# Kernel optimization log

Measured on AMD Instinct MI355X. Metric: run time of the kernel, lower is better.

Reference implementation:

```python
import jax, jax.numpy as jnp
import numpy as np

B = 4096          # SDE paths (batch_size)
N = 50            # timesteps
DIM = 1
DIM_W = 1
DT = 0.02         # T = 1.0
SIGMA_C = 0.5     # constant diffusion coefficient sigma(t,y)
H = 64            # MLP hidden width ('Default' architecture)
NHID = 3          # three 64->64 hidden layers after the input layer


def _mlp(t, y, Win, bin_, Whid, bhid, Wout, bout):
    # FCnet([2,64,64,64,64,1]) with Sine activation on concat([t, y])
    h = jnp.sin(jnp.concatenate([t, y], axis=-1) @ Win + bin_)
    for i in range(NHID):
        h = jnp.sin(h @ Whid[i] + bhid[i])
    return h @ Wout + bout


def setup_inputs() -> dict:
    key = jax.random.key(0)
    ks = jax.random.split(key, 16)
    def w(k, shape, fan):
        return jax.random.normal(k, shape, jnp.float32) / np.float32(np.sqrt(fan))
    inp = {}
    for p, i in (("Y", 0), ("q", 8)):
        inp[p + "_Win"] = w(ks[i], (2, H), 2)
        inp[p + "_bin"] = jnp.zeros((H,), jnp.float32)
        inp[p + "_Whid"] = w(ks[i + 1], (NHID, H, H), H)
        inp[p + "_bhid"] = jnp.zeros((NHID, H), jnp.float32)
        inp[p + "_Wout"] = w(ks[i + 2], (H, 1), H)
        inp[p + "_bout"] = jnp.zeros((1,), jnp.float32)
    inp["y0_param"] = jnp.ones((1,), jnp.float32)
    inp["dW"] = jax.random.normal(ks[7], (N, B, DIM_W), jnp.float32)  # unit normals; scaled by sqrt(dt) inside reference
    return inp


def _fbsnn_loss(y0_param, Y_Win, Y_bin, Y_Whid, Y_bhid, Y_Wout, Y_bout,
                q_Win, q_bin, q_Whid, q_bhid, q_Wout, q_bout, dW):
    Y_net = lambda t, y: _mlp(t, y, Y_Win, Y_bin, Y_Whid, Y_bhid, Y_Wout, Y_bout)
    q_net = lambda t, y: _mlp(t, y, q_Win, q_bin, q_Whid, q_bhid, q_Wout, q_bout)

    def Y_and_grad(t, y):
        # autograd.grad(Y, y, ones_like(Y)) -> per-sample dY/dy since Y is [B,1]
        Yv, vjp = jax.vjp(lambda yy: Y_net(t, yy), y)
        return Yv, vjp(jnp.ones_like(Yv))[0]

    dWs = dW * np.float32(np.sqrt(DT))             # [N, B, dim_W]
    t0 = jnp.zeros((B, 1), dW.dtype)
    y0 = jnp.tile(y0_param[None, :], (B, 1))       # y0.repeat(batch,1)
    Y0, dY0 = Y_and_grad(t0, y0)

    def step(carry, dW_n):
        t, y, Yv, dYv, loss = carry
        q = q_net(t, y)                                          # control
        sig = jnp.full((B, DIM, DIM_W), SIGMA_C, dW_n.dtype)     # sigma(t,y)
        y1 = y + q * DT + jnp.einsum('bij,bj->bi', sig, dW_n)    # mu = q
        Z = jnp.einsum('bij,bj->bi', sig, dYv)                   # bmm(sigma, dY)
        t1 = t + DT
        Y1, dY1 = Y_and_grad(t1, y1)
        f = q ** 2                                               # generator(y,q)
        Y1_tilde = Yv - f * DT + Z * dW_n
        loss = loss + jnp.mean((Y1 - Y1_tilde) ** 2)
        return (t1, y1, Y1, dY1, loss), None

    carry0 = (t0, y0, Y0, dY0, jnp.zeros((), dW.dtype))
    (tN, yN, YN, dYN, res_loss), _ = jax.lax.scan(step, carry0, dWs)

    g = lambda yy: jnp.sum(yy ** 2, axis=-1, keepdims=True)      # terminal_cost(y)
    term, vjp_g = jax.vjp(g, yN)
    term_grad = vjp_g(jnp.ones_like(term))[0]
    return (res_loss
            + jnp.mean((YN - term) ** 2)
            + jnp.mean((dYN - term_grad) ** 2))


def reference(y0_param, Y_Win, Y_bin, Y_Whid, Y_bhid, Y_Wout, Y_bout,
              q_Win, q_bin, q_Whid, q_bhid, q_Wout, q_bout, dW):
    return _fbsnn_loss(y0_param, Y_Win, Y_bin, Y_Whid, Y_bhid, Y_Wout, Y_bout,
                       q_Win, q_bin, q_Whid, q_bhid, q_Wout, q_bout, dW)
```

## Files before the change

kernel.cpp:

```cpp
#include <hip/hip_runtime.h>


#define NPATH   4096
#define NSTEP   50
#define DT_F    0.02f
#define SQRT_DT 0.14142136f
#define SIGMA_F 0.5f
#define INV2PI  0.15915494309189535f
#define TWOPI_F 6.28318530717958648f

#define GRID_N   128
#define GRID_INV 8.0f
#define GRID_DY  0.125f

#define NPROD_Q 25
#define NPROD_Y 26
#define NCONS   64
#define NBLK    (51 + NCONS)
#define PPB     64

#define QG_FLOATS  (NSTEP * GRID_N)
#define YD_FLOATS  (2 * (NSTEP + 1) * GRID_N)

#define MAGIC 0x5AB1C0DEu

#define FR_AIN(t)     (t)
#define FR_AH(L,t,kk) (4 + (L)*8 + (t)*2 + (kk))
#define FR_AOUT(kk)   (28 + (kk))
#define FR_BIN(t)     (30 + (t))
#define FR_BHD(L,t)   (34 + (L)*4 + (t))
#define FR_BOUT       46

#define WS_DONE 0
#define WS_QG   64
#define WS_YD   (WS_QG + QG_FLOATS)
#define WS_PAIR (WS_YD + YD_FLOATS)

#define L_QG    0
#define L_YD    QG_FLOATS
#define L_DW    (L_YD + YD_FLOATS)
#define SMEM_FLOATS (L_DW + NSTEP * PPB)
#define SMEM_BYTES  (SMEM_FLOATS * 4)

typedef __attribute__((ext_vector_type(8)))  short s16x8;
typedef __attribute__((ext_vector_type(4)))  float f32x4;
typedef __attribute__((ext_vector_type(4)))  float float4v;
typedef __attribute__((ext_vector_type(2)))  float float2v;

#if __has_builtin(__builtin_amdgcn_cvt_pk_bf16_f32)
__device__ __forceinline__ unsigned pkbf(float a, float b) {
    auto r = __builtin_amdgcn_cvt_pk_bf16_f32(a, b);
    unsigned u; __builtin_memcpy(&u, &r, 4); return u;
}
#else
__device__ __forceinline__ unsigned pkbf(float a, float b) {
    unsigned ua = __float_as_uint(a), ub = __float_as_uint(b);
    ua += 0x7fffu + ((ua >> 16) & 1u);
    ub += 0x7fffu + ((ub >> 16) & 1u);
    return (ua >> 16) | (ub & 0xffff0000u);
}
#endif

__device__ __forceinline__ s16x8 frag4(unsigned a, unsigned b, unsigned c, unsigned d) {
    union { unsigned u[4]; s16x8 s; } x;
    x.u[0] = a; x.u[1] = b; x.u[2] = c; x.u[3] = d;
    return x.s;
}

__device__ __forceinline__ float sinrev(float x) {
#if __has_builtin(__builtin_amdgcn_sinf)
    return __builtin_amdgcn_sinf(x);
#else
    return __sinf(x * TWOPI_F);
#endif
}
__device__ __forceinline__ float cosrev(float x) {
#if __has_builtin(__builtin_amdgcn_cosf)
    return __builtin_amdgcn_cosf(x);
#else
    return __cosf(x * TWOPI_F);
#endif
}

__device__ __forceinline__ int slot16(int t, int r) {
    return (t < 2) ? 8 * (r >> 2) + 4 * t + (r & 3)
                   : 32 + 8 * (r >> 2) + 4 * (t - 2) + (r & 3);
}

__device__ __forceinline__ void build_half(
    int sec, int half, const float* __restrict__ Win, const float* __restrict__ bin,
    const float* __restrict__ Whid, const float* __restrict__ bhid,
    const float* __restrict__ Wout, const float* __restrict__ bo,
    int qd, int m, char* fbl)
{
    const int t0 = 2 * half;
    if (sec == 0) {
#pragma unroll
        for (int t = t0; t < t0 + 2; ++t) {
            const int uo = slot16(t, m);
            unsigned w0 = 0;
            if (qd == 0) w0 = pkbf(INV2PI * Win[uo], INV2PI * Win[64 + uo]);
            *reinterpret_cast<s16x8*>(fbl + FR_AIN(t) * 1024) = frag4(w0, 0u, 0u, 0u);
            f32x4 bi;
#pragma unroll
            for (int i = 0; i < 4; ++i) bi[i] = INV2PI * bin[slot16(t, 4 * qd + i)];
            *reinterpret_cast<f32x4*>(fbl + FR_BIN(t) * 1024) = bi;
        }
        if (half == 0) {
#pragma unroll
            for (int kk = 0; kk < 2; ++kk) {
                unsigned w[4] = {0u, 0u, 0u, 0u};
                if (m == 0) {
#pragma unroll
                    for (int j2 = 0; j2 < 4; ++j2) {
                        int e0 = 32 * kk + 8 * qd + 2 * j2;
                        w[j2] = pkbf(Wout[e0], Wout[e0 + 1]);
                    }
                }
                *reinterpret_cast<s16x8*>(fbl + FR_AOUT(kk) * 1024) = frag4(w[0], w[1], w[2], w[3]);
            }
            f32x4 bo4 = {bo[0], 0.0f, 0.0f, 0.0f};
            *reinterpret_cast<f32x4*>(fbl + FR_BOUT * 1024) = bo4;
        }
    } else {
        const int L = sec - 1;
#pragma unroll
        for (int t = t0; t < t0 + 2; ++t) {
            const int uo = slot16(t, m);
            const float* W = Whid + L * 4096 + uo;
#pragma unroll
            for (int kk = 0; kk < 2; ++kk) {
                unsigned w[4];
#pragma unroll
                for (int j2 = 0; j2 < 4; ++j2) {
                    int e0 = 32 * kk + 8 * qd + 2 * j2;
                    w[j2] = pkbf(INV2PI * W[e0 * 64], INV2PI * W[(e0 + 1) * 64]);
                }
                *reinterpret_cast<s16x8*>(fbl + FR_AH(L, t, kk) * 1024) = frag4(w[0], w[1], w[2], w[3]);
            }
            f32x4 bh;
#pragma unroll
            for (int i = 0; i < 4; ++i) bh[i] = INV2PI * bhid[L * 64 + slot16(t, 4 * qd + i)];
            *reinterpret_cast<f32x4*>(fbl + FR_BHD(L, t) * 1024) = bh;
        }
    }
}

__device__ __forceinline__ void trans16(const f32x4* C, s16x8& B0, s16x8& B1) {
    float a[4][4];
#pragma unroll
    for (int t = 0; t < 4; ++t)
#pragma unroll
        for (int i = 0; i < 4; ++i) a[t][i] = sinrev(C[t][i]);
    B0 = frag4(pkbf(a[0][0], a[0][1]), pkbf(a[0][2], a[0][3]),
               pkbf(a[1][0], a[1][1]), pkbf(a[1][2], a[1][3]));
    B1 = frag4(pkbf(a[2][0], a[2][1]), pkbf(a[2][2], a[2][3]),
               pkbf(a[3][0], a[3][1]), pkbf(a[3][2], a[3][3]));
}

__device__ __forceinline__ void trans16t(const f32x4* Cf, const f32x4* Ct,
                                         s16x8& Bf0, s16x8& Bf1,
                                         s16x8& Bt0, s16x8& Bt1)
{
    float s[4][4], d[4][4];
#pragma unroll
    for (int t = 0; t < 4; ++t)
#pragma unroll
        for (int i = 0; i < 4; ++i) {
            float cf = Cf[t][i];
            s[t][i] = sinrev(cf);
            d[t][i] = cosrev(cf) * (TWOPI_F * Ct[t][i]);
        }
    Bf0 = frag4(pkbf(s[0][0], s[0][1]), pkbf(s[0][2], s[0][3]),
                pkbf(s[1][0], s[1][1]), pkbf(s[1][2], s[1][3]));
    Bf1 = frag4(pkbf(s[2][0], s[2][1]), pkbf(s[2][2], s[2][3]),
                pkbf(s[3][0], s[3][1]), pkbf(s[3][2], s[3][3]));
    Bt0 = frag4(pkbf(d[0][0], d[0][1]), pkbf(d[0][2], d[0][3]),
                pkbf(d[1][0], d[1][1]), pkbf(d[1][2], d[1][3]));
    Bt1 = frag4(pkbf(d[2][0], d[2][1]), pkbf(d[2][2], d[2][3]),
                pkbf(d[3][0], d[3][1]), pkbf(d[3][2], d[3][3]));
}

__device__ __forceinline__ float grid_ylo(const float* __restrict__ y0p) {
    return floorf(y0p[0] * 8.0f) * 0.125f - 8.0f;
}

__device__ __forceinline__ float eval16_q(const char* fbl, const s16x8& Bty) {
    const f32x4 zc = {0.0f, 0.0f, 0.0f, 0.0f};
    f32x4 C[4];
#pragma unroll
    for (int t = 0; t < 4; ++t) {
        const s16x8 a  = *reinterpret_cast<const s16x8*>(fbl + FR_AIN(t) * 1024);
        const f32x4 bi = *reinterpret_cast<const f32x4*>(fbl + FR_BIN(t) * 1024);
        C[t] = __builtin_amdgcn_mfma_f32_16x16x32_bf16(a, Bty, bi, 0, 0, 0);
    }
    s16x8 B0, B1;
    trans16(C, B0, B1);
#pragma unroll
    for (int L = 0; L < 3; ++L) {
#pragma unroll
        for (int t = 0; t < 4; ++t) {
            const s16x8 a0 = *reinterpret_cast<const s16x8*>(fbl + FR_AH(L, t, 0) * 1024);
            const s16x8 a1 = *reinterpret_cast<const s16x8*>(fbl + FR_AH(L, t, 1) * 1024);
            const f32x4 bh = *reinterpret_cast<const f32x4*>(fbl + FR_BHD(L, t) * 1024);
            f32x4 c = __builtin_amdgcn_mfma_f32_16x16x32_bf16(a0, B0, bh, 0, 0, 0);
            C[t]    = __builtin_amdgcn_mfma_f32_16x16x32_bf16(a1, B1, c, 0, 0, 0);
        }
        trans16(C, B0, B1);
    }
    const s16x8 o0 = *reinterpret_cast<const s16x8*>(fbl + FR_AOUT(0) * 1024);
    const s16x8 o1 = *reinterpret_cast<const s16x8*>(fbl + FR_AOUT(1) * 1024);
    f32x4 Co = __builtin_amdgcn_mfma_f32_16x16x32_bf16(o0, B0, zc, 0, 0, 0);
    Co = __builtin_amdgcn_mfma_f32_16x16x32_bf16(o1, B1, Co, 0, 0, 0);
    return Co[0] + *reinterpret_cast<const float*>(fbl + FR_BOUT * 1024);
}

__device__ __forceinline__ void eval16t(const char* fbl, const s16x8& Bty,
                                        const s16x8& Btn, float& Yv, float& dYv) {
    const f32x4 zc = {0.0f, 0.0f, 0.0f, 0.0f};
    f32x4 Cf[4], Ct[4];
#pragma unroll
    for (int t = 0; t < 4; ++t) {
        const s16x8 a  = *reinterpret_cast<const s16x8*>(fbl + FR_AIN(t) * 1024);
        const f32x4 bi = *reinterpret_cast<const f32x4*>(fbl + FR_BIN(t) * 1024);
        Cf[t] = __builtin_amdgcn_mfma_f32_16x16x32_bf16(a, Bty, bi, 0, 0, 0);
        Ct[t] = __builtin_amdgcn_mfma_f32_16x16x32_bf16(a, Btn, zc, 0, 0, 0);
    }
    s16x8 bf0, bf1, bt0, bt1;
    trans16t(Cf, Ct, bf0, bf1, bt0, bt1);
#pragma unroll
    for (int L = 0; L < 3; ++L) {
#pragma unroll
        for (int t = 0; t < 4; ++t) {
            const s16x8 a0 = *reinterpret_cast<const s16x8*>(fbl + FR_AH(L, t, 0) * 1024);
            const s16x8 a1 = *reinterpret_cast<const s16x8*>(fbl + FR_AH(L, t, 1) * 1024);
            const f32x4 bh = *reinterpret_cast<const f32x4*>(fbl + FR_BHD(L, t) * 1024);
            f32x4 c = __builtin_amdgcn_mfma_f32_16x16x32_bf16(a0, bf0, bh, 0, 0, 0);
            Cf[t]   = __builtin_amdgcn_mfma_f32_16x16x32_bf16(a1, bf1, c, 0, 0, 0);
            f32x4 z = __builtin_amdgcn_mfma_f32_16x16x32_bf16(a0, bt0, zc, 0, 0, 0);
            Ct[t]   = __builtin_amdgcn_mfma_f32_16x16x32_bf16(a1, bt1, z, 0, 0, 0);
        }
        trans16t(Cf, Ct, bf0, bf1, bt0, bt1);
    }
    const s16x8 o0 = *reinterpret_cast<const s16x8*>(fbl + FR_AOUT(0) * 1024);
    const s16x8 o1 = *reinterpret_cast<const s16x8*>(fbl + FR_AOUT(1) * 1024);
    f32x4 Cof = __builtin_amdgcn_mfma_f32_16x16x32_bf16(o0, bf0, zc, 0, 0, 0);
    Cof = __builtin_amdgcn_mfma_f32_16x16x32_bf16(o1, bf1, Cof, 0, 0, 0);
    f32x4 Cot = __builtin_amdgcn_mfma_f32_16x16x32_bf16(o0, bt0, zc, 0, 0, 0);
    Cot = __builtin_amdgcn_mfma_f32_16x16x32_bf16(o1, bt1, Cot, 0, 0, 0);
    Yv  = Cof[0] + *reinterpret_cast<const float*>(fbl + FR_BOUT * 1024);
    dYv = Cot[0];
}

__device__ __forceinline__ float cm4(float q0, float q1, float q2, float q3, float fr) {
    return q1 + 0.5f * fr * ((q2 - q0)
             + fr * ((2.0f * q0 - 5.0f * q1 + 4.0f * q2 - q3)
             + fr * (3.0f * (q1 - q2) + q3 - q0)));
}


extern "C" __global__ void __launch_bounds__(1024, 4)
fbsnn_one(const float* __restrict__ Y_Win, const float* __restrict__ Y_bin,
          const float* __restrict__ Y_Whid, const float* __restrict__ Y_bhid,
          const float* __restrict__ Y_Wout, const float* __restrict__ Y_bout,
          const float* __restrict__ q_Win, const float* __restrict__ q_bin,
          const float* __restrict__ q_Whid, const float* __restrict__ q_bhid,
          const float* __restrict__ q_Wout, const float* __restrict__ q_bout,
          const float* __restrict__ y0p, const float* __restrict__ dW,
          float* __restrict__ ws, float* __restrict__ out)
{
    extern __shared__ __align__(16) float sf[];

    int* done = (int*)ws;
    unsigned long long* pairs = (unsigned long long*)(ws + WS_PAIR);

    const int tid = (int)threadIdx.x;
    const int wv  = tid >> 6;
    const int l   = tid & 63;
    const int qd  = l >> 4;
    const int mm  = l & 15;
    const int blk = (int)blockIdx.x;

    const float ylo = grid_ylo(y0p);

    if (blk < 51) {
        const bool is_q = (blk < NPROD_Q);
        char* fbl = (char*)sf + l * 16;

        if (wv < 8) {
            if (is_q)
                build_half(wv >> 1, wv & 1, q_Win, q_bin, q_Whid, q_bhid,
                           q_Wout, q_bout, qd, mm, fbl);
            else
                build_half(wv >> 1, wv & 1, Y_Win, Y_bin, Y_Whid, Y_bhid,
                           Y_Wout, Y_bout, qd, mm, fbl);
        }
        __syncthreads();

        const int rib  = wv >> 3;
        const int colg = wv & 7;
        const int col  = 16 * colg + mm;
        const int n    = is_q ? (2 * blk + rib) : (2 * (blk - NPROD_Q) + rib);
        const bool valid = is_q ? (n < NSTEP) : (n <= NSTEP);
        if (valid) {
            const float tt = n * DT_F;
            const float yg = ylo + (float)col * GRID_DY;
            const s16x8 Bty = frag4((qd == 0) ? pkbf(tt, yg) : 0u, 0u, 0u, 0u);
            if (is_q) {
                const float qv = eval16_q(fbl, Bty);
                if (qd == 0) ws[WS_QG + n * GRID_N + col] = qv;
            } else {
                const s16x8 Btn = frag4((qd == 0) ? pkbf(0.0f, 1.0f) : 0u, 0u, 0u, 0u);
                float Yv, dYv;
                eval16t(fbl, Bty, Btn, Yv, dYv);
                if (qd == 0) {
                    float2v p; p.x = Yv; p.y = dYv;
                    ((float2v*)(ws + WS_YD))[n * GRID_N + col] = p;
                }
            }
        }
        __syncthreads();

        if (tid == 0) {
            __threadfence();
            __hip_atomic_store(&done[blk], (int)MAGIC, __ATOMIC_RELAXED,
                               __HIP_MEMORY_SCOPE_AGENT);
        }
        return;
    }

    const int cid = blk - 51;
    float* qg  = sf + L_QG;
    float* dWb = sf + L_DW;
    const int ts = tid - 64;

    if (wv != 0 && ts < 800) {
        const int r = ts >> 4, j4 = ts & 15;
        ((float4v*)dWb)[ts] =
            *(const float4v*)(dW + r * NPATH + cid * PPB + j4 * 4);
    }

    if (wv == 0) {
        if (l < NPROD_Q)
            while (__hip_atomic_load(&done[l], __ATOMIC_RELAXED,
                                     __HIP_MEMORY_SCOPE_AGENT) != (int)MAGIC)
                __builtin_amdgcn_s_sleep(1);
        __threadfence();
    }
    __syncthreads();

    if (wv != 0) {
#pragma unroll
        for (int k = 0; k < 2; ++k) {
            const int idx = ts + k * 960;
            if (idx < 1600)
                ((float4v*)qg)[idx] = ((const float4v*)(ws + WS_QG))[idx];
        }
    } else {
        if (l < NPROD_Y)
            while (__hip_atomic_load(&done[NPROD_Q + l], __ATOMIC_RELAXED,
                                     __HIP_MEMORY_SCOPE_AGENT) != (int)MAGIC)
                __builtin_amdgcn_s_sleep(1);
        __threadfence();
    }
    __syncthreads();

    {
#pragma unroll
        for (int k = 0; k < 4; ++k) {
            const int idx = tid + k * 1024;
            if (idx < (YD_FLOATS / 4))
                ((float4v*)(sf + L_YD))[idx] = ((const float4v*)(ws + WS_YD))[idx];
        }
    }
    __syncthreads();

    if (wv != 0) return;

    const float2v* yd = (const float2v*)(sf + L_YD);

    float y   = y0p[0];
    float acc = 0.0f;
    float Yp = 0.0f, dYp = 0.0f, qp = 0.0f, dwp = 0.0f;

    for (int n = 0; n < NSTEP; ++n) {
        const float dwv = dWb[n * PPB + l];

        float u = (y - ylo) * GRID_INV;
        u = fminf(fmaxf(u, 1.0f), 125.999f);
        int i = (int)u;
        if (i > 125) i = 125;
        const float fr = u - (float)i;

        const float* qr = qg + n * GRID_N + i;
        const float qn = cm4(qr[-1], qr[0], qr[1], qr[2], fr);

        const float2v* yr = yd + n * GRID_N + (i - 1);
        const float2v p0 = yr[0], p1 = yr[1], p2 = yr[2], p3 = yr[3];
        const float Yn  = cm4(p0.x, p1.x, p2.x, p3.x, fr);
        const float dYn = cm4(p0.y, p1.y, p2.y, p3.y, fr);

        if (n) {
            const float r = Yn - (fmaf(-qp * qp, DT_F, Yp)
                                  + (SIGMA_F * dYp) * (dwp * SQRT_DT));
            acc = fmaf(r, r, acc);
        }
        qp = qn; Yp = Yn; dYp = dYn; dwp = dwv;
        y = fmaf(qn, DT_F, y) + SIGMA_F * (dwv * SQRT_DT);
    }
    {
        float u = (y - ylo) * GRID_INV;
        u = fminf(fmaxf(u, 1.0f), 125.999f);
        int i = (int)u;
        if (i > 125) i = 125;
        const float fr = u - (float)i;
        const float2v* yr = yd + NSTEP * GRID_N + (i - 1);
        const float2v p0 = yr[0], p1 = yr[1], p2 = yr[2], p3 = yr[3];
        const float Y50  = cm4(p0.x, p1.x, p2.x, p3.x, fr);
        const float dY50 = cm4(p0.y, p1.y, p2.y, p3.y, fr);
        const float r = Y50 - (fmaf(-qp * qp, DT_F, Yp)
                               + (SIGMA_F * dYp) * (dwp * SQRT_DT));
        acc = fmaf(r, r, acc);
        const float r1 = Y50 - y * y;
        const float r2 = dY50 - 2.0f * y;
        acc = fmaf(r1, r1, fmaf(r2, r2, acc));
    }

#pragma unroll
    for (int off = 32; off > 0; off >>= 1) acc += __shfl_down(acc, off, 64);

    if (l == 0) {
        const unsigned long long pv =
            ((unsigned long long)MAGIC << 32) |
            (unsigned long long)__float_as_uint(acc);
        __hip_atomic_store(&pairs[cid], pv, __ATOMIC_RELAXED,
                           __HIP_MEMORY_SCOPE_AGENT);
    }
    if (cid == 0) {
        unsigned long long v;
        while ((unsigned)((v = __hip_atomic_load(&pairs[l], __ATOMIC_RELAXED,
                        __HIP_MEMORY_SCOPE_AGENT)) >> 32) != MAGIC)
            __builtin_amdgcn_s_sleep(1);
        float s = __uint_as_float((unsigned)(v & 0xffffffffu));
#pragma unroll
        for (int off = 32; off > 0; off >>= 1) s += __shfl_down(s, off, 64);
        if (l == 0) out[0] = s * (1.0f / (float)NPATH);
    }
}


extern "C" void kernel_launch(void* const* d_in, const int* in_sizes, int n_in,
                              void* d_out, int out_size, void* d_ws, size_t ws_size,
                              hipStream_t stream)
{
    const float* Y_Win  = (const float*)d_in[0];
    const float* Y_bin  = (const float*)d_in[1];
    const float* Y_Whid = (const float*)d_in[2];
    const float* Y_bhid = (const float*)d_in[3];
    const float* Y_Wout = (const float*)d_in[4];
    const float* Y_bout = (const float*)d_in[5];
    const float* q_Win  = (const float*)d_in[6];
    const float* q_bin  = (const float*)d_in[7];
    const float* q_Whid = (const float*)d_in[8];
    const float* q_bhid = (const float*)d_in[9];
    const float* q_Wout = (const float*)d_in[10];
    const float* q_bout = (const float*)d_in[11];
    const float* y0p    = (const float*)d_in[12];
    const float* dW     = (const float*)d_in[13];

    fbsnn_one<<<dim3(NBLK), dim3(1024), SMEM_BYTES, stream>>>(
        Y_Win, Y_bin, Y_Whid, Y_bhid, Y_Wout, Y_bout,
        q_Win, q_bin, q_Whid, q_bhid, q_Wout, q_bout,
        y0p, dW, (float*)d_ws, (float*)d_out);
}
```

Baseline: 102.8 us.

## Merge producer and consumer blocks into one 64-block grid

Each of the 64 blocks now consumes one path chunk, and the first 51 blocks also build the q/Y lookup grids. This replaces the earlier layout of 51 producer blocks plus 64 separate consumer blocks. dW is staged into shared memory by the upper waves while the producer waves build fragments, and the q and Y/dY grids are copied in one combined loop. The per-step dW load is prefetched one iteration ahead. The change cuts the block count and overlaps staging with production, but the consumer work in producer blocks now runs only after their own production finishes, and correctness relies on all 64 blocks being co-resident for the spin-waits.

```diff
diff --git a/kernel.cpp b/kernel.cpp
--- a/kernel.cpp
+++ b/kernel.cpp
@@ -14,9 +14,7 @@
 #define GRID_DY  0.125f
 
 #define NPROD_Q 25
-#define NPROD_Y 26
-#define NCONS   64
-#define NBLK    (51 + NCONS)
+#define NBLK    64
 #define PPB     64
 
 #define QG_FLOATS  (NSTEP * GRID_N)
@@ -38,6 +36,7 @@
 
 #define L_QG    0
 #define L_YD    QG_FLOATS
+#define L_FB    L_YD
 #define L_DW    (L_YD + YD_FLOATS)
 #define SMEM_FLOATS (L_DW + NSTEP * PPB)
 #define SMEM_BYTES  (SMEM_FLOATS * 4)
@@ -270,6 +269,8 @@
           float* __restrict__ ws, float* __restrict__ out)
 {
     extern __shared__ __align__(16) float sf[];
+    float* qg  = sf + L_QG;
+    float* dWb = sf + L_DW;
 
     int* done = (int*)ws;
     unsigned long long* pairs = (unsigned long long*)(ws + WS_PAIR);
@@ -281,13 +282,13 @@
     const int mm  = l & 15;
     const int blk = (int)blockIdx.x;
 
+    const bool prod = (blk < 51);
+    const bool is_q = (blk < NPROD_Q);
     const float ylo = grid_ylo(y0p);
 
-    if (blk < 51) {
-        const bool is_q = (blk < NPROD_Q);
-        char* fbl = (char*)sf + l * 16;
-
-        if (wv < 8) {
+    if (wv < 8) {
+        if (prod) {
+            char* fbl = (char*)(sf + L_FB) + l * 16;
             if (is_q)
                 build_half(wv >> 1, wv & 1, q_Win, q_bin, q_Whid, q_bhid,
                            q_Wout, q_bout, qd, mm, fbl);
@@ -295,8 +296,20 @@
                 build_half(wv >> 1, wv & 1, Y_Win, Y_bin, Y_Whid, Y_bhid,
                            Y_Wout, Y_bout, qd, mm, fbl);
         }
-        __syncthreads();
-
+    } else {
+        const int ts = tid - 512;
+#pragma unroll
+        for (int k = 0; k < 2; ++k) {
+            const int idx = ts + k * 512;
+            if (idx < 800)
+                ((float4v*)dWb)[idx] =
+                    *(const float4v*)(dW + (idx >> 4) * NPATH + blk * PPB + (idx & 15) * 4);
+        }
+    }
+    __syncthreads();
+
+    if (prod) {
+        const char* fbl = (const char*)(sf + L_FB) + l * 16;
         const int rib  = wv >> 3;
         const int colg = wv & 7;
         const int col  = 16 * colg + mm;
@@ -320,24 +333,11 @@
             }
         }
         __syncthreads();
-
         if (tid == 0) {
             __threadfence();
             __hip_atomic_store(&done[blk], (int)MAGIC, __ATOMIC_RELAXED,
                                __HIP_MEMORY_SCOPE_AGENT);
         }
-        return;
-    }
-
-    const int cid = blk - 51;
-    float* qg  = sf + L_QG;
-    float* dWb = sf + L_DW;
-    const int ts = tid - 64;
-
-    if (wv != 0 && ts < 800) {
-        const int r = ts >> 4, j4 = ts & 15;
-        ((float4v*)dWb)[ts] =
-            *(const float4v*)(dW + r * NPATH + cid * PPB + j4 * 4);
     }
 
     if (wv == 0) {
@@ -345,19 +345,7 @@
             while (__hip_atomic_load(&done[l], __ATOMIC_RELAXED,
                                      __HIP_MEMORY_SCOPE_AGENT) != (int)MAGIC)
                 __builtin_amdgcn_s_sleep(1);
-        __threadfence();
-    }
-    __syncthreads();
-
-    if (wv != 0) {
-#pragma unroll
-        for (int k = 0; k < 2; ++k) {
-            const int idx = ts + k * 960;
-            if (idx < 1600)
-                ((float4v*)qg)[idx] = ((const float4v*)(ws + WS_QG))[idx];
-        }
-    } else {
-        if (l < NPROD_Y)
+        if (l < 26)
             while (__hip_atomic_load(&done[NPROD_Q + l], __ATOMIC_RELAXED,
                                      __HIP_MEMORY_SCOPE_AGENT) != (int)MAGIC)
                 __builtin_amdgcn_s_sleep(1);
@@ -365,13 +353,11 @@
     }
     __syncthreads();
 
-    {
-#pragma unroll
-        for (int k = 0; k < 4; ++k) {
-            const int idx = tid + k * 1024;
-            if (idx < (YD_FLOATS / 4))
-                ((float4v*)(sf + L_YD))[idx] = ((const float4v*)(ws + WS_YD))[idx];
-        }
+#pragma unroll
+    for (int k = 0; k < 5; ++k) {
+        const int idx = tid + k * 1024;
+        if (idx < (L_DW / 4))
+            ((float4v*)sf)[idx] = ((const float4v*)(ws + WS_QG))[idx];
     }
     __syncthreads();
 
@@ -382,9 +368,10 @@
     float y   = y0p[0];
     float acc = 0.0f;
     float Yp = 0.0f, dYp = 0.0f, qp = 0.0f, dwp = 0.0f;
+    float dwv = dWb[l];
 
     for (int n = 0; n < NSTEP; ++n) {
-        const float dwv = dWb[n * PPB + l];
+        const float dw_next = (n + 1 < NSTEP) ? dWb[(n + 1) * PPB + l] : 0.0f;
 
         float u = (y - ylo) * GRID_INV;
         u = fminf(fmaxf(u, 1.0f), 125.999f);
@@ -407,6 +394,7 @@
         }
         qp = qn; Yp = Yn; dYp = dYn; dwp = dwv;
         y = fmaf(qn, DT_F, y) + SIGMA_F * (dwv * SQRT_DT);
+        dwv = dw_next;
     }
     {
         float u = (y - ylo) * GRID_INV;
@@ -433,10 +421,10 @@
         const unsigned long long pv =
             ((unsigned long long)MAGIC << 32) |
             (unsigned long long)__float_as_uint(acc);
-        __hip_atomic_store(&pairs[cid], pv, __ATOMIC_RELAXED,
+        __hip_atomic_store(&pairs[blk], pv, __ATOMIC_RELAXED,
                            __HIP_MEMORY_SCOPE_AGENT);
     }
-    if (cid == 0) {
+    if (blk == 0) {
         unsigned long long v;
         while ((unsigned)((v = __hip_atomic_load(&pairs[l], __ATOMIC_RELAXED,
                         __HIP_MEMORY_SCOPE_AGENT)) >> 32) != MAGIC)
```

Measured after the change: 98.50 us. 1.04x faster.
